# Kernel tuning notes

Hardware: AMD Instinct MI355X
Metric: run time of the kernel (lower is better)

## Reference

```python
import jax, jax.numpy as jnp
import numpy as np

DIM = 1024
N_HEADS = 16
HEAD_DIM = DIM // N_HEADS


def setup_inputs() -> dict:
    key = jax.random.key(0)
    ks = jax.random.split(key, 7)
    s = 1.0 / np.sqrt(DIM)
    return {
        "hidden_states": jax.random.normal(ks[0], (1, 4096, DIM), dtype=jnp.float32),
        "Wq": jax.random.uniform(ks[1], (DIM, DIM), jnp.float32, -s, s),
        "bq": jax.random.uniform(ks[2], (DIM,), jnp.float32, -s, s),
        "Wk": jax.random.uniform(ks[3], (DIM, DIM), jnp.float32, -s, s),
        "bk": jax.random.uniform(ks[4], (DIM,), jnp.float32, -s, s),
        "Wv": jax.random.uniform(ks[5], (DIM, DIM), jnp.float32, -s, s),
        "bv": jax.random.uniform(ks[6], (DIM,), jnp.float32, -s, s),
    }


def _split_heads(x):
    # [B, S, DIM] -> [B, H, S, HEAD_DIM]
    b, s, _ = x.shape
    return x.reshape(b, s, N_HEADS, HEAD_DIM).transpose(0, 2, 1, 3)


def reference(hidden_states, Wq, bq, Wk, bk, Wv, bv):
    q = _split_heads(hidden_states @ Wq + bq)
    k = _split_heads(hidden_states @ Wk + bk)
    v = _split_heads(hidden_states @ Wv + bv)
    scores = jnp.einsum("bhqd,bhkd->bhqk", q, k) / np.sqrt(HEAD_DIM).astype(np.float32)
    probs = jax.nn.softmax(scores, axis=-1)  # dropout prob = 0 -> identity
    ctx = jnp.einsum("bhqk,bhkd->bhqd", probs, v)
    b, h, s, d = ctx.shape
    return ctx.transpose(0, 2, 1, 3).reshape(b, s, h * d)
```

## Files before the change

### kernel.cpp

```cpp
#include <hip/hip_runtime.h>
#include <hip/hip_bf16.h>

#define S_LEN 4096
#define DIM   1024
#define NH    16
#define HD    64

typedef unsigned short u16;
typedef short  bf16x8 __attribute__((ext_vector_type(8)));
typedef float  f32x4  __attribute__((ext_vector_type(4)));

__device__ __forceinline__ u16 f2bf(float f){
  union { float f; unsigned u; } x; x.f = f;
  unsigned u = x.u;
  return (u16)((u + 0x7FFFu + ((u >> 16) & 1u)) >> 16);
}
__device__ __forceinline__ unsigned pk2(float a, float b){
  union { __hip_bfloat162 h; unsigned u; } x;
  x.h = __float22bfloat162_rn(float2{a, b});
  return x.u;
}
__device__ __forceinline__ void ld2lds16(const u16* g, u16* l){
  __builtin_amdgcn_global_load_lds((const __attribute__((address_space(1))) void*)g,
                                   (__attribute__((address_space(3))) void*)l, 16, 0, 0);
}

#define QSCALE 0.1803368801111204f

__global__ __launch_bounds__(256) void fill_sentinel(float* __restrict__ out, int n){
  int i = blockIdx.x * 256 + threadIdx.x;
  if (i < n) out[i] = 77.0f;
}

__global__ __launch_bounds__(256) void conv_x(const float* __restrict__ X, u16* __restrict__ Xb){
  size_t i = ((size_t)blockIdx.x * 256 + threadIdx.x) * 8;
  float4 v0 = *(const float4*)(X + i);
  float4 v1 = *(const float4*)(X + i + 4);
  uint4 w;
  w.x = pk2(v0.x, v0.y); w.y = pk2(v0.z, v0.w);
  w.z = pk2(v1.x, v1.y); w.w = pk2(v1.z, v1.w);
  *(uint4*)(Xb + i) = w;
}

__global__ __launch_bounds__(256) void transpose_w(
    const float* __restrict__ W0, const float* __restrict__ W1, const float* __restrict__ W2,
    u16* __restrict__ Wt)
{
  const float* W = blockIdx.z==0 ? W0 : blockIdx.z==1 ? W1 : W2;
  u16* T = Wt + (size_t)blockIdx.z * DIM * DIM;
  __shared__ __align__(16) u16 tile[64*72];
  int k0 = blockIdx.x*64, n0 = blockIdx.y*64;
  int t = threadIdx.x;
  #pragma unroll
  for (int i = 0; i < 4; ++i){
    int idx = t + i*256;
    int row = idx >> 4, col4 = (idx & 15) * 4;
    float4 v = *(const float4*)(W + (size_t)(k0+row)*DIM + n0 + col4);
    tile[(col4+0)*72 + row] = f2bf(v.x);
    tile[(col4+1)*72 + row] = f2bf(v.y);
    tile[(col4+2)*72 + row] = f2bf(v.z);
    tile[(col4+3)*72 + row] = f2bf(v.w);
  }
  __syncthreads();
  #pragma unroll
  for (int i = 0; i < 2; ++i){
    int idx = t + i*256;
    int n = idx >> 3, k16 = (idx & 7) * 8;
    *(int4*)(T + (size_t)(n0+n)*DIM + k0 + k16) = *(const int4*)(tile + n*72 + k16);
  }
}

__device__ __forceinline__ void qkv_epilogue(
    int z, int m0, int n0, int wm, int wn, int quad, int l15,
    const f32x4 acc[4][4], const float* bias,
    u16* __restrict__ qb, u16* __restrict__ kf_out, u16* __restrict__ vf_out)
{
  #pragma unroll
  for (int nt=0; nt<4; ++nt){
    int n = n0 + wn + nt*16 + l15;
    float bv = bias[n];
    int h = n >> 6, d = n & 63;
    #pragma unroll
    for (int mt=0; mt<4; ++mt){
      int mb = m0 + wm + mt*16 + quad*4;
      f32x4 c = acc[mt][nt];
      if (z == 0){
        #pragma unroll
        for (int r=0; r<4; ++r)
          qb[(size_t)(mb + r)*DIM + n] = f2bf((c[r] + bv) * QSCALE);
      } else if (z == 1){
        int half = d >> 5, quadk = (d >> 3) & 3, j = d & 7;
        #pragma unroll
        for (int r=0; r<4; ++r){
          int s = mb + r;
          size_t idx = ((((size_t)h*256 + (s >> 4))*2 + half)*64 + quadk*16 + (s & 15))*8 + j;
          kf_out[idx] = f2bf(c[r] + bv);
        }
      } else {
        int kt64 = mb >> 6;
        int kn   = (mb >> 4) & 3;
        int qsl  = (mb >> 2) & 3;
        int h2   = kn >> 1;
        int jj0  = (kn & 1) * 4;
        int dt = d >> 4, dl = d & 15;
        size_t base = (((((size_t)h*64 + kt64)*4 + dt)*2 + h2)*64 + qsl*16 + dl)*8 + jj0;
        ushort4 p;
        p.x = f2bf(c[0]+bv); p.y = f2bf(c[1]+bv);
        p.z = f2bf(c[2]+bv); p.w = f2bf(c[3]+bv);
        *(ushort4*)(vf_out + base) = p;
      }
    }
  }
}

__global__ __launch_bounds__(256) void qkv_gemm_fast(
    const u16* __restrict__ Xbf, const u16* __restrict__ Wt,
    const float* __restrict__ b0, const float* __restrict__ b1, const float* __restrict__ b2,
    u16* __restrict__ qb, u16* __restrict__ kf_out, u16* __restrict__ vf_out)
{
  int z = blockIdx.z;
  const u16* Wz = Wt + (size_t)z * DIM * DIM;
  const float* bias = z==0 ? b0 : z==1 ? b1 : b2;

  __shared__ __align__(16) u16 As[128*32];
  __shared__ __align__(16) u16 Bs[128*32];

  int m0 = blockIdx.x * 128, n0 = blockIdx.y * 128;
  int t = threadIdx.x, wave = t >> 6, lane = t & 63, quad = lane >> 4, l15 = lane & 15;
  int wm = (wave >> 1) * 64, wn = (wave & 1) * 64;

  f32x4 acc[4][4];
  #pragma unroll
  for (int i=0;i<4;++i)
    #pragma unroll
    for (int j=0;j<4;++j) acc[i][j] = (f32x4){0.f,0.f,0.f,0.f};

  int srow = wave*32 + (lane >> 2);
  int skc  = (lane & 3) * 8;
  const u16* gA0 = Xbf + (size_t)(m0 + srow)*DIM + skc;
  const u16* gA1 = gA0 + (size_t)16*DIM;
  const u16* gB0 = Wz  + (size_t)(n0 + srow)*DIM + skc;
  const u16* gB1 = gB0 + (size_t)16*DIM;
  u16* lA0 = As + srow*32 + skc;
  u16* lA1 = lA0 + 16*32;
  u16* lB0 = Bs + srow*32 + skc;
  u16* lB1 = lB0 + 16*32;

  for (int kt = 0; kt < 32; ++kt){
    int ko = kt * 32;
    __syncthreads();
    ld2lds16(gA0 + ko, lA0);
    ld2lds16(gA1 + ko, lA1);
    ld2lds16(gB0 + ko, lB0);
    ld2lds16(gB1 + ko, lB1);
    __syncthreads();
    bf16x8 af[4], bfr[4];
    #pragma unroll
    for (int mt=0; mt<4; ++mt) af[mt]  = *(const bf16x8*)(As + (wm + mt*16 + l15)*32 + quad*8);
    #pragma unroll
    for (int nt=0; nt<4; ++nt) bfr[nt] = *(const bf16x8*)(Bs + (wn + nt*16 + l15)*32 + quad*8);
    #pragma unroll
    for (int mt=0; mt<4; ++mt)
      #pragma unroll
      for (int nt=0; nt<4; ++nt)
        acc[mt][nt] = __builtin_amdgcn_mfma_f32_16x16x32_bf16(af[mt], bfr[nt], acc[mt][nt], 0, 0, 0);
  }
  qkv_epilogue(z, m0, n0, wm, wn, quad, l15, acc, bias, qb, kf_out, vf_out);
}

__global__ __launch_bounds__(256) void qkv_gemm_legacy(
    const float* __restrict__ X,
    const float* __restrict__ Wq, const float* __restrict__ Wk, const float* __restrict__ Wv,
    const float* __restrict__ b0, const float* __restrict__ b1, const float* __restrict__ b2,
    u16* __restrict__ qb, u16* __restrict__ kf_out, u16* __restrict__ vf_out)
{
  int z = blockIdx.z;
  const float* W    = z==0 ? Wq : z==1 ? Wk : Wv;
  const float* bias = z==0 ? b0 : z==1 ? b1 : b2;

  __shared__ __align__(16) u16 As[128*40];
  __shared__ __align__(16) u16 Bs[128*40];

  int m0 = blockIdx.x * 128, n0 = blockIdx.y * 128;
  int t = threadIdx.x, wave = t >> 6, lane = t & 63, quad = lane >> 4, l15 = lane & 15;
  int wm = (wave >> 1) * 64, wn = (wave & 1) * 64;

  f32x4 acc[4][4];
  #pragma unroll
  for (int i=0;i<4;++i)
    #pragma unroll
    for (int j=0;j<4;++j) acc[i][j] = (f32x4){0.f,0.f,0.f,0.f};

  int sr = t >> 2, sc = (t & 3) * 8;
  const float* gA0 = X + (size_t)(m0 + sr) * DIM + sc;
  const float* gA1 = X + (size_t)(m0 + 64 + sr) * DIM + sc;
  int br = t >> 3, bc = (t & 7) * 16;
  const float* gW = W + (size_t)br * DIM + n0 + bc;

  for (int kt = 0; kt < 32; ++kt){
    int ko = kt * 32;
    float4 a00 = *(const float4*)(gA0 + ko);
    float4 a01 = *(const float4*)(gA0 + ko + 4);
    float4 a10 = *(const float4*)(gA1 + ko);
    float4 a11 = *(const float4*)(gA1 + ko + 4);
    float4 w0  = *(const float4*)(gW + (size_t)ko*DIM);
    float4 w1  = *(const float4*)(gW + (size_t)ko*DIM + 4);
    float4 w2  = *(const float4*)(gW + (size_t)ko*DIM + 8);
    float4 w3  = *(const float4*)(gW + (size_t)ko*DIM + 12);
    int4 pa0, pa1;
    pa0.x = pk2(a00.x,a00.y); pa0.y = pk2(a00.z,a00.w);
    pa0.z = pk2(a01.x,a01.y); pa0.w = pk2(a01.z,a01.w);
    pa1.x = pk2(a10.x,a10.y); pa1.y = pk2(a10.z,a10.w);
    pa1.z = pk2(a11.x,a11.y); pa1.w = pk2(a11.z,a11.w);
    u16 wb[16];
    wb[0]=f2bf(w0.x); wb[1]=f2bf(w0.y); wb[2]=f2bf(w0.z); wb[3]=f2bf(w0.w);
    wb[4]=f2bf(w1.x); wb[5]=f2bf(w1.y); wb[6]=f2bf(w1.z); wb[7]=f2bf(w1.w);
    wb[8]=f2bf(w2.x); wb[9]=f2bf(w2.y); wb[10]=f2bf(w2.z); wb[11]=f2bf(w2.w);
    wb[12]=f2bf(w3.x); wb[13]=f2bf(w3.y); wb[14]=f2bf(w3.z); wb[15]=f2bf(w3.w);
    __syncthreads();
    *(int4*)(As + sr*40 + sc)      = pa0;
    *(int4*)(As + (64+sr)*40 + sc) = pa1;
    #pragma unroll
    for (int j=0;j<16;++j) Bs[(bc+j)*40 + br] = wb[j];
    __syncthreads();
    bf16x8 af[4], bfr[4];
    #pragma unroll
    for (int mt=0; mt<4; ++mt) af[mt]  = *(const bf16x8*)(As + (wm + mt*16 + l15)*40 + quad*8);
    #pragma unroll
    for (int nt=0; nt<4; ++nt) bfr[nt] = *(const bf16x8*)(Bs + (wn + nt*16 + l15)*40 + quad*8);
    #pragma unroll
    for (int mt=0; mt<4; ++mt)
      #pragma unroll
      for (int nt=0; nt<4; ++nt)
        acc[mt][nt] = __builtin_amdgcn_mfma_f32_16x16x32_bf16(af[mt], bfr[nt], acc[mt][nt], 0, 0, 0);
  }
  qkv_epilogue(z, m0, n0, wm, wn, quad, l15, acc, bias, qb, kf_out, vf_out);
}

__global__ __launch_bounds__(256, 2) void attn(
    const u16* __restrict__ Qb, const u16* __restrict__ Kf,
    const u16* __restrict__ Vf, float* __restrict__ out)
{
  int fid = blockIdx.x;
  int xcd  = fid & 7;
  int hpar = (fid >> 3) & 1;
  int qb   = fid >> 4;
  int h    = xcd*2 + hpar;

  int t = threadIdx.x, wave = t >> 6, lane = t & 63, quad = lane >> 4, l15 = lane & 15;
  int q0 = qb * 128 + wave * 32;

  __shared__ __align__(16) u16 Ks0[4096], Ks1[4096], Vs0[4096], Vs1[4096];

  const u16* Kfh = Kf + (size_t)h * 262144;
  const u16* Vfh = Vf + (size_t)h * 262144;

  bf16x8 qf[2][2];
  #pragma unroll
  for (int qs=0; qs<2; ++qs){
    const u16* Qp = Qb + (size_t)(q0 + qs*16 + l15)*DIM + h*HD;
    qf[qs][0] = *(const bf16x8*)(Qp + quad*8);
    qf[qs][1] = *(const bf16x8*)(Qp + 32 + quad*8);
  }

  f32x4 O[2][4];
  #pragma unroll
  for (int qs=0; qs<2; ++qs)
    #pragma unroll
    for (int dt=0; dt<4; ++dt) O[qs][dt] = (f32x4){0.f,0.f,0.f,0.f};
  float lsum[2] = {0.f, 0.f};

#define STAGE(KS, VS, T)                                                         \
  do {                                                                           \
    const u16* kg_ = Kfh + (size_t)(T)*4096 + t*8;                               \
    ld2lds16(kg_,        KS + t*8);                                              \
    ld2lds16(kg_ + 2048, KS + t*8 + 2048);                                       \
    const u16* vg_ = Vfh + (size_t)(T)*4096 + t*8;                               \
    ld2lds16(vg_,        VS + t*8);                                              \
    ld2lds16(vg_ + 2048, VS + t*8 + 2048);                                       \
  } while(0)

#define ATTN_COMPUTE(KS, VS)                                                     \
  do {                                                                           \
    bf16x8 kfr[4][2], vfr[4][2];                                                 \
    _Pragma("unroll")                                                            \
    for (int kn=0; kn<4; ++kn)                                                   \
      _Pragma("unroll")                                                          \
      for (int hf=0; hf<2; ++hf)                                                 \
        kfr[kn][hf] = *(const bf16x8*)(KS + (kn*2+hf)*512 + lane*8);             \
    _Pragma("unroll")                                                            \
    for (int dt=0; dt<4; ++dt)                                                   \
      _Pragma("unroll")                                                          \
      for (int c2=0; c2<2; ++c2)                                                 \
        vfr[dt][c2] = *(const bf16x8*)(VS + (dt*2+c2)*512 + lane*8);             \
    f32x4 st[2][4];                                                              \
    _Pragma("unroll")                                                            \
    for (int qs=0; qs<2; ++qs)                                                   \
      _Pragma("unroll")                                                          \
      for (int kn=0; kn<4; ++kn){                                                \
        f32x4 zz = (f32x4){0.f,0.f,0.f,0.f};                                     \
        zz = __builtin_amdgcn_mfma_f32_16x16x32_bf16(kfr[kn][0], qf[qs][0], zz, 0,0,0); \
        zz = __builtin_amdgcn_mfma_f32_16x16x32_bf16(kfr[kn][1], qf[qs][1], zz, 0,0,0); \
        st[qs][kn] = zz;                                                         \
      }                                                                          \
    _Pragma("unroll")                                                            \
    for (int qs=0; qs<2; ++qs){                                                  \
      float ls = 0.f;                                                            \
      _Pragma("unroll")                                                          \
      for (int kn=0; kn<4; ++kn)                                                 \
        _Pragma("unroll")                                                        \
        for (int r=0; r<4; ++r){                                                 \
          float p = __builtin_amdgcn_exp2f(st[qs][kn][r]);                       \
          st[qs][kn][r] = p; ls += p;                                            \
        }                                                                        \
      lsum[qs] += ls;                                                            \
      union { uint4 u; bf16x8 v; } pf0, pf1;                                     \
      pf0.u.x = pk2(st[qs][0][0], st[qs][0][1]);                                 \
      pf0.u.y = pk2(st[qs][0][2], st[qs][0][3]);                                 \
      pf0.u.z = pk2(st[qs][1][0], st[qs][1][1]);                                 \
      pf0.u.w = pk2(st[qs][1][2], st[qs][1][3]);                                 \
      pf1.u.x = pk2(st[qs][2][0], st[qs][2][1]);                                 \
      pf1.u.y = pk2(st[qs][2][2], st[qs][2][3]);                                 \
      pf1.u.z = pk2(st[qs][3][0], st[qs][3][1]);                                 \
      pf1.u.w = pk2(st[qs][3][2], st[qs][3][3]);                                 \
      _Pragma("unroll")                                                          \
      for (int dt=0; dt<4; ++dt){                                                \
        f32x4 o = O[qs][dt];                                                     \
        o = __builtin_amdgcn_mfma_f32_16x16x32_bf16(vfr[dt][0], pf0.v, o, 0,0,0); \
        o = __builtin_amdgcn_mfma_f32_16x16x32_bf16(vfr[dt][1], pf1.v, o, 0,0,0); \
        O[qs][dt] = o;                                                           \
      }                                                                          \
    }                                                                            \
  } while(0)

  STAGE(Ks0, Vs0, 0);
  __syncthreads();

  for (int kt = 0; kt < 64; kt += 2){
    STAGE(Ks1, Vs1, kt+1);
    ATTN_COMPUTE(Ks0, Vs0);
    __syncthreads();
    if (kt < 62) STAGE(Ks0, Vs0, kt+2);
    ATTN_COMPUTE(Ks1, Vs1);
    __syncthreads();
  }
#undef ATTN_COMPUTE
#undef STAGE

  #pragma unroll
  for (int qs=0; qs<2; ++qs){
    float l = lsum[qs];
    l += __shfl_xor(l, 16, 64);
    l += __shfl_xor(l, 32, 64);
    float inv = 1.0f / l;
    int query = q0 + qs*16 + l15;
    #pragma unroll
    for (int dt=0; dt<4; ++dt){
      float4 v;
      v.x = O[qs][dt][0]*inv; v.y = O[qs][dt][1]*inv;
      v.z = O[qs][dt][2]*inv; v.w = O[qs][dt][3]*inv;
      *(float4*)(out + (size_t)query*DIM + h*HD + dt*16 + quad*4) = v;
    }
  }
}

extern "C" void kernel_launch(void* const* d_in, const int* in_sizes, int n_in,
                              void* d_out, int out_size, void* d_ws, size_t ws_size,
                              hipStream_t stream)
{
  const float* X  = (const float*)d_in[0];
  const float* Wq = (const float*)d_in[1];
  const float* bq = (const float*)d_in[2];
  const float* Wk = (const float*)d_in[3];
  const float* bk = (const float*)d_in[4];
  const float* Wv = (const float*)d_in[5];
  const float* bv = (const float*)d_in[6];
  float* out = (float*)d_out;
  u16*   ws  = (u16*)d_ws;

  const size_t SD = (size_t)S_LEN * DIM;
  const size_t need_fast = (4*SD + 3*(size_t)DIM*DIM) * sizeof(u16);
  const size_t need_min  = (size_t)24 * 1024 * 1024;

  if (ws_size >= need_fast){
    u16* xbf = ws;
    u16* wt  = xbf + SD;
    u16* qb  = wt + 3*(size_t)DIM*DIM;
    u16* kf  = qb + SD;
    u16* vf  = kf + SD;
    conv_x       <<<dim3((int)(SD/8/256)), 256, 0, stream>>>(X, xbf);
    transpose_w  <<<dim3(16,16,3), 256, 0, stream>>>(Wq, Wk, Wv, wt);
    qkv_gemm_fast<<<dim3(32, 8, 3), 256, 0, stream>>>(xbf, wt, bq, bk, bv, qb, kf, vf);
    attn         <<<dim3(512), 256, 0, stream>>>(qb, kf, vf, out);
  } else if (ws_size >= need_min){
    u16* qb = ws;
    u16* kf = qb + SD;
    u16* vf = kf + SD;
    qkv_gemm_legacy<<<dim3(32, 8, 3), 256, 0, stream>>>(X, Wq, Wk, Wv, bq, bk, bv, qb, kf, vf);
    attn           <<<dim3(512), 256, 0, stream>>>(qb, kf, vf, out);
  } else {
    fill_sentinel<<<(out_size + 255)/256, 256, 0, stream>>>(out, out_size);
  }
}
```

Baseline: 210.9 us.

## Halve queries per wave in attention to double grid and occupancy

Each attention wave now processes one 16-query slice instead of two, so a block covers 64 queries and the grid grows to 1024 blocks, with launch bounds raised to allow 4 blocks per CU. This lowers register pressure and raises occupancy to hide latency of the exp and MFMA chain. In exchange, each staged K/V tile is reused by half as many queries, doubling K/V load and LDS traffic per unit of work.

```diff
diff --git a/kernel.cpp b/kernel.cpp
--- a/kernel.cpp
+++ b/kernel.cpp
@@ -237,7 +237,7 @@
   qkv_epilogue(z, m0, n0, wm, wn, quad, l15, acc, bias, qb, kf_out, vf_out);
 }
 
-__global__ __launch_bounds__(256, 2) void attn(
+__global__ __launch_bounds__(256, 4) void attn(
     const u16* __restrict__ Qb, const u16* __restrict__ Kf,
     const u16* __restrict__ Vf, float* __restrict__ out)
 {
@@ -248,27 +248,24 @@
   int h    = xcd*2 + hpar;
 
   int t = threadIdx.x, wave = t >> 6, lane = t & 63, quad = lane >> 4, l15 = lane & 15;
-  int q0 = qb * 128 + wave * 32;
+  int q0 = qb * 64 + wave * 16;
 
   __shared__ __align__(16) u16 Ks0[4096], Ks1[4096], Vs0[4096], Vs1[4096];
 
   const u16* Kfh = Kf + (size_t)h * 262144;
   const u16* Vfh = Vf + (size_t)h * 262144;
 
-  bf16x8 qf[2][2];
-  #pragma unroll
-  for (int qs=0; qs<2; ++qs){
-    const u16* Qp = Qb + (size_t)(q0 + qs*16 + l15)*DIM + h*HD;
-    qf[qs][0] = *(const bf16x8*)(Qp + quad*8);
-    qf[qs][1] = *(const bf16x8*)(Qp + 32 + quad*8);
-  }
-
-  f32x4 O[2][4];
-  #pragma unroll
-  for (int qs=0; qs<2; ++qs)
-    #pragma unroll
-    for (int dt=0; dt<4; ++dt) O[qs][dt] = (f32x4){0.f,0.f,0.f,0.f};
-  float lsum[2] = {0.f, 0.f};
+  bf16x8 qf[2];
+  {
+    const u16* Qp = Qb + (size_t)(q0 + l15)*DIM + h*HD;
+    qf[0] = *(const bf16x8*)(Qp + quad*8);
+    qf[1] = *(const bf16x8*)(Qp + 32 + quad*8);
+  }
+
+  f32x4 O[4];
+  #pragma unroll
+  for (int dt=0; dt<4; ++dt) O[dt] = (f32x4){0.f,0.f,0.f,0.f};
+  float lsum = 0.f;
 
 #define STAGE(KS, VS, T)                                                         \
   do {                                                                           \
@@ -293,43 +290,38 @@
       _Pragma("unroll")                                                          \
       for (int c2=0; c2<2; ++c2)                                                 \
         vfr[dt][c2] = *(const bf16x8*)(VS + (dt*2+c2)*512 + lane*8);             \
-    f32x4 st[2][4];                                                              \
-    _Pragma("unroll")                                                            \
-    for (int qs=0; qs<2; ++qs)                                                   \
+    f32x4 st[4];                                                                 \
+    _Pragma("unroll")                                                            \
+    for (int kn=0; kn<4; ++kn){                                                  \
+      f32x4 zz = (f32x4){0.f,0.f,0.f,0.f};                                       \
+      zz = __builtin_amdgcn_mfma_f32_16x16x32_bf16(kfr[kn][0], qf[0], zz, 0,0,0); \
+      zz = __builtin_amdgcn_mfma_f32_16x16x32_bf16(kfr[kn][1], qf[1], zz, 0,0,0); \
+      st[kn] = zz;                                                               \
+    }                                                                            \
+    float ls = 0.f;                                                              \
+    _Pragma("unroll")                                                            \
+    for (int kn=0; kn<4; ++kn)                                                   \
       _Pragma("unroll")                                                          \
-      for (int kn=0; kn<4; ++kn){                                                \
-        f32x4 zz = (f32x4){0.f,0.f,0.f,0.f};                                     \
-        zz = __builtin_amdgcn_mfma_f32_16x16x32_bf16(kfr[kn][0], qf[qs][0], zz, 0,0,0); \
-        zz = __builtin_amdgcn_mfma_f32_16x16x32_bf16(kfr[kn][1], qf[qs][1], zz, 0,0,0); \
-        st[qs][kn] = zz;                                                         \
+      for (int r=0; r<4; ++r){                                                   \
+        float p = __builtin_amdgcn_exp2f(st[kn][r]);                             \
+        st[kn][r] = p; ls += p;                                                  \
       }                                                                          \
-    _Pragma("unroll")                                                            \
-    for (int qs=0; qs<2; ++qs){                                                  \
-      float ls = 0.f;                                                            \
-      _Pragma("unroll")                                                          \
-      for (int kn=0; kn<4; ++kn)                                                 \
-        _Pragma("unroll")                                                        \
-        for (int r=0; r<4; ++r){                                                 \
-          float p = __builtin_amdgcn_exp2f(st[qs][kn][r]);                       \
-          st[qs][kn][r] = p; ls += p;                                            \
-        }                                                                        \
-      lsum[qs] += ls;                                                            \
-      union { uint4 u; bf16x8 v; } pf0, pf1;                                     \
-      pf0.u.x = pk2(st[qs][0][0], st[qs][0][1]);                                 \
-      pf0.u.y = pk2(st[qs][0][2], st[qs][0][3]);                                 \
-      pf0.u.z = pk2(st[qs][1][0], st[qs][1][1]);                                 \
-      pf0.u.w = pk2(st[qs][1][2], st[qs][1][3]);                                 \
-      pf1.u.x = pk2(st[qs][2][0], st[qs][2][1]);                                 \
-      pf1.u.y = pk2(st[qs][2][2], st[qs][2][3]);                                 \
-      pf1.u.z = pk2(st[qs][3][0], st[qs][3][1]);                                 \
-      pf1.u.w = pk2(st[qs][3][2], st[qs][3][3]);                                 \
-      _Pragma("unroll")                                                          \
-      for (int dt=0; dt<4; ++dt){                                                \
-        f32x4 o = O[qs][dt];                                                     \
-        o = __builtin_amdgcn_mfma_f32_16x16x32_bf16(vfr[dt][0], pf0.v, o, 0,0,0); \
-        o = __builtin_amdgcn_mfma_f32_16x16x32_bf16(vfr[dt][1], pf1.v, o, 0,0,0); \
-        O[qs][dt] = o;                                                           \
-      }                                                                          \
+    lsum += ls;                                                                  \
+    union { uint4 u; bf16x8 v; } pf0, pf1;                                       \
+    pf0.u.x = pk2(st[0][0], st[0][1]);                                           \
+    pf0.u.y = pk2(st[0][2], st[0][3]);                                           \
+    pf0.u.z = pk2(st[1][0], st[1][1]);                                           \
+    pf0.u.w = pk2(st[1][2], st[1][3]);                                           \
+    pf1.u.x = pk2(st[2][0], st[2][1]);                                           \
+    pf1.u.y = pk2(st[2][2], st[2][3]);                                           \
+    pf1.u.z = pk2(st[3][0], st[3][1]);                                           \
+    pf1.u.w = pk2(st[3][2], st[3][3]);                                           \
+    _Pragma("unroll")                                                            \
+    for (int dt=0; dt<4; ++dt){                                                  \
+      f32x4 o = O[dt];                                                           \
+      o = __builtin_amdgcn_mfma_f32_16x16x32_bf16(vfr[dt][0], pf0.v, o, 0,0,0);  \
+      o = __builtin_amdgcn_mfma_f32_16x16x32_bf16(vfr[dt][1], pf1.v, o, 0,0,0);  \
+      O[dt] = o;                                                                 \
     }                                                                            \
   } while(0)
 
@@ -347,18 +339,17 @@
 #undef ATTN_COMPUTE
 #undef STAGE
 
-  #pragma unroll
-  for (int qs=0; qs<2; ++qs){
-    float l = lsum[qs];
+  {
+    float l = lsum;
     l += __shfl_xor(l, 16, 64);
     l += __shfl_xor(l, 32, 64);
     float inv = 1.0f / l;
-    int query = q0 + qs*16 + l15;
+    int query = q0 + l15;
     #pragma unroll
     for (int dt=0; dt<4; ++dt){
       float4 v;
-      v.x = O[qs][dt][0]*inv; v.y = O[qs][dt][1]*inv;
-      v.z = O[qs][dt][2]*inv; v.w = O[qs][dt][3]*inv;
+      v.x = O[dt][0]*inv; v.y = O[dt][1]*inv;
+      v.z = O[dt][2]*inv; v.w = O[dt][3]*inv;
       *(float4*)(out + (size_t)query*DIM + h*HD + dt*16 + quad*4) = v;
     }
   }
@@ -391,13 +382,13 @@
     conv_x       <<<dim3((int)(SD/8/256)), 256, 0, stream>>>(X, xbf);
     transpose_w  <<<dim3(16,16,3), 256, 0, stream>>>(Wq, Wk, Wv, wt);
     qkv_gemm_fast<<<dim3(32, 8, 3), 256, 0, stream>>>(xbf, wt, bq, bk, bv, qb, kf, vf);
-    attn         <<<dim3(512), 256, 0, stream>>>(qb, kf, vf, out);
+    attn         <<<dim3(1024), 256, 0, stream>>>(qb, kf, vf, out);
   } else if (ws_size >= need_min){
     u16* qb = ws;
     u16* kf = qb + SD;
     u16* vf = kf + SD;
     qkv_gemm_legacy<<<dim3(32, 8, 3), 256, 0, stream>>>(X, Wq, Wk, Wv, bq, bk, bv, qb, kf, vf);
-    attn           <<<dim3(512), 256, 0, stream>>>(qb, kf, vf, out);
+    attn           <<<dim3(1024), 256, 0, stream>>>(qb, kf, vf, out);
   } else {
     fill_sentinel<<<(out_size + 255)/256, 256, 0, stream>>>(out, out_size);
   }
```

After: 213.9 us. Within noise of the previous version (+1.4%).

## Software-pipeline attention loop to overlap QK of next tile with PV of previous

Applied to the files above, without the earlier changes.

Restructures the attention inner loop so that the QK^T MFMAs for tile t+1 are issued alongside the PV MFMAs for tile t, with exp/pack and V-fragment loads done one stage ahead in registers. The aim is to hide the dependency chain between score computation, exp, and the PV matmul, and to let matrix work overlap with transcendental work. It adds double-buffered register state (scores, packed probs, V fragments), which raises register pressure and could cut occupancy.

```diff
diff --git a/kernel.cpp b/kernel.cpp
--- a/kernel.cpp
+++ b/kernel.cpp
@@ -280,20 +280,14 @@
     ld2lds16(vg_ + 2048, VS + t*8 + 2048);                                       \
   } while(0)
 
-#define ATTN_COMPUTE(KS, VS)                                                     \
+#define QK_BLOCK(KS, ST)                                                         \
   do {                                                                           \
-    bf16x8 kfr[4][2], vfr[4][2];                                                 \
+    bf16x8 kfr[4][2];                                                            \
     _Pragma("unroll")                                                            \
     for (int kn=0; kn<4; ++kn)                                                   \
       _Pragma("unroll")                                                          \
       for (int hf=0; hf<2; ++hf)                                                 \
-        kfr[kn][hf] = *(const bf16x8*)(KS + (kn*2+hf)*512 + lane*8);             \
-    _Pragma("unroll")                                                            \
-    for (int dt=0; dt<4; ++dt)                                                   \
-      _Pragma("unroll")                                                          \
-      for (int c2=0; c2<2; ++c2)                                                 \
-        vfr[dt][c2] = *(const bf16x8*)(VS + (dt*2+c2)*512 + lane*8);             \
-    f32x4 st[2][4];                                                              \
+        kfr[kn][hf] = *(const bf16x8*)((KS) + (kn*2+hf)*512 + lane*8);           \
     _Pragma("unroll")                                                            \
     for (int qs=0; qs<2; ++qs)                                                   \
       _Pragma("unroll")                                                          \
@@ -301,8 +295,25 @@
         f32x4 zz = (f32x4){0.f,0.f,0.f,0.f};                                     \
         zz = __builtin_amdgcn_mfma_f32_16x16x32_bf16(kfr[kn][0], qf[qs][0], zz, 0,0,0); \
         zz = __builtin_amdgcn_mfma_f32_16x16x32_bf16(kfr[kn][1], qf[qs][1], zz, 0,0,0); \
-        st[qs][kn] = zz;                                                         \
+        ST[qs][kn] = zz;                                                         \
       }                                                                          \
+  } while(0)
+
+#define PV_BLOCK(PF, VFR)                                                        \
+  do {                                                                           \
+    _Pragma("unroll")                                                            \
+    for (int qs=0; qs<2; ++qs)                                                   \
+      _Pragma("unroll")                                                          \
+      for (int dt=0; dt<4; ++dt){                                                \
+        f32x4 o = O[qs][dt];                                                     \
+        o = __builtin_amdgcn_mfma_f32_16x16x32_bf16(VFR[dt][0], PF[qs][0].v, o, 0,0,0); \
+        o = __builtin_amdgcn_mfma_f32_16x16x32_bf16(VFR[dt][1], PF[qs][1].v, o, 0,0,0); \
+        O[qs][dt] = o;                                                           \
+      }                                                                          \
+  } while(0)
+
+#define EXP_PACK(ST, PF)                                                         \
+  do {                                                                           \
     _Pragma("unroll")                                                            \
     for (int qs=0; qs<2; ++qs){                                                  \
       float ls = 0.f;                                                            \
@@ -310,42 +321,73 @@
       for (int kn=0; kn<4; ++kn)                                                 \
         _Pragma("unroll")                                                        \
         for (int r=0; r<4; ++r){                                                 \
-          float p = __builtin_amdgcn_exp2f(st[qs][kn][r]);                       \
-          st[qs][kn][r] = p; ls += p;                                            \
+          float p = __builtin_amdgcn_exp2f(ST[qs][kn][r]);                       \
+          ST[qs][kn][r] = p; ls += p;                                            \
         }                                                                        \
       lsum[qs] += ls;                                                            \
-      union { uint4 u; bf16x8 v; } pf0, pf1;                                     \
-      pf0.u.x = pk2(st[qs][0][0], st[qs][0][1]);                                 \
-      pf0.u.y = pk2(st[qs][0][2], st[qs][0][3]);                                 \
-      pf0.u.z = pk2(st[qs][1][0], st[qs][1][1]);                                 \
-      pf0.u.w = pk2(st[qs][1][2], st[qs][1][3]);                                 \
-      pf1.u.x = pk2(st[qs][2][0], st[qs][2][1]);                                 \
-      pf1.u.y = pk2(st[qs][2][2], st[qs][2][3]);                                 \
-      pf1.u.z = pk2(st[qs][3][0], st[qs][3][1]);                                 \
-      pf1.u.w = pk2(st[qs][3][2], st[qs][3][3]);                                 \
-      _Pragma("unroll")                                                          \
-      for (int dt=0; dt<4; ++dt){                                                \
-        f32x4 o = O[qs][dt];                                                     \
-        o = __builtin_amdgcn_mfma_f32_16x16x32_bf16(vfr[dt][0], pf0.v, o, 0,0,0); \
-        o = __builtin_amdgcn_mfma_f32_16x16x32_bf16(vfr[dt][1], pf1.v, o, 0,0,0); \
-        O[qs][dt] = o;                                                           \
-      }                                                                          \
+      PF[qs][0].u.x = pk2(ST[qs][0][0], ST[qs][0][1]);                           \
+      PF[qs][0].u.y = pk2(ST[qs][0][2], ST[qs][0][3]);                           \
+      PF[qs][0].u.z = pk2(ST[qs][1][0], ST[qs][1][1]);                           \
+      PF[qs][0].u.w = pk2(ST[qs][1][2], ST[qs][1][3]);                           \
+      PF[qs][1].u.x = pk2(ST[qs][2][0], ST[qs][2][1]);                           \
+      PF[qs][1].u.y = pk2(ST[qs][2][2], ST[qs][2][3]);                           \
+      PF[qs][1].u.z = pk2(ST[qs][3][0], ST[qs][3][1]);                           \
+      PF[qs][1].u.w = pk2(ST[qs][3][2], ST[qs][3][3]);                           \
     }                                                                            \
   } while(0)
 
+#define LOADV(VFR, VS)                                                           \
+  do {                                                                           \
+    _Pragma("unroll")                                                            \
+    for (int dt=0; dt<4; ++dt)                                                   \
+      _Pragma("unroll")                                                          \
+      for (int c2=0; c2<2; ++c2)                                                 \
+        VFR[dt][c2] = *(const bf16x8*)((VS) + (dt*2+c2)*512 + lane*8);           \
+  } while(0)
+
+  typedef union { uint4 u; bf16x8 v; } pfu;
+  pfu pfA[2][2], pfB[2][2];
+  bf16x8 vfrA[4][2], vfrB[4][2];
+  f32x4 stA[2][4], stB[2][4];
+
   STAGE(Ks0, Vs0, 0);
   __syncthreads();
-
-  for (int kt = 0; kt < 64; kt += 2){
-    STAGE(Ks1, Vs1, kt+1);
-    ATTN_COMPUTE(Ks0, Vs0);
-    __syncthreads();
-    if (kt < 62) STAGE(Ks0, Vs0, kt+2);
-    ATTN_COMPUTE(Ks1, Vs1);
-    __syncthreads();
-  }
-#undef ATTN_COMPUTE
+  STAGE(Ks1, Vs1, 1);
+  QK_BLOCK(Ks0, stA);
+  EXP_PACK(stA, pfA);
+  LOADV(vfrA, Vs0);
+  __syncthreads();
+
+  for (int i = 0; i < 31; ++i){
+    int t1 = 2*i + 1;
+    {
+      STAGE(Ks0, Vs0, t1+1);
+      QK_BLOCK(Ks1, stB);
+      PV_BLOCK(pfA, vfrA);
+      EXP_PACK(stB, pfB);
+      LOADV(vfrB, Vs1);
+      __syncthreads();
+    }
+    {
+      STAGE(Ks1, Vs1, t1+2);
+      QK_BLOCK(Ks0, stA);
+      PV_BLOCK(pfB, vfrB);
+      EXP_PACK(stA, pfA);
+      LOADV(vfrA, Vs0);
+      __syncthreads();
+    }
+  }
+  QK_BLOCK(Ks1, stB);
+  PV_BLOCK(pfA, vfrA);
+  EXP_PACK(stB, pfB);
+  LOADV(vfrB, Vs1);
+  PV_BLOCK(pfB, vfrB);
+
 #undef STAGE
+#undef QK_BLOCK
+#undef PV_BLOCK
+#undef EXP_PACK
+#undef LOADV
 
   #pragma unroll
   for (int qs=0; qs<2; ++qs){
```

After: 208.4 us. Within noise of the previous version (-1.2%).

## Stagger waves between QK/exp and PV phases with software pipelining and setprio

Applied to the files above, without the earlier changes.

Splits the attention tile compute into QK+exp, V load and PV steps. Half of the waves, chosen by wave parity XOR block index, defer the PV of the previous tile so it runs before the current QK. This staggers which phase different waves are in, so exp/VALU work in one wave can overlap MFMA work in another. It also raises wave priority around the MFMA sections. The cost is extra registers for the carried P fragments and V fragments, which may hurt occupancy at launch bounds of 2 blocks per CU, and the control flow becomes divergent per wave.

```diff
diff --git a/kernel.cpp b/kernel.cpp
--- a/kernel.cpp
+++ b/kernel.cpp
@@ -249,6 +249,7 @@
 
   int t = threadIdx.x, wave = t >> 6, lane = t & 63, quad = lane >> 4, l15 = lane & 15;
   int q0 = qb * 128 + wave * 32;
+  int dg = (wave ^ (fid >> 8)) & 1;
 
   __shared__ __align__(16) u16 Ks0[4096], Ks1[4096], Vs0[4096], Vs1[4096];
 
@@ -269,6 +270,8 @@
     #pragma unroll
     for (int dt=0; dt<4; ++dt) O[qs][dt] = (f32x4){0.f,0.f,0.f,0.f};
   float lsum[2] = {0.f, 0.f};
+
+  typedef union { uint4 u; bf16x8 v; } pfu;
 
 #define STAGE(KS, VS, T)                                                         \
   do {                                                                           \
@@ -280,20 +283,16 @@
     ld2lds16(vg_ + 2048, VS + t*8 + 2048);                                       \
   } while(0)
 
-#define ATTN_COMPUTE(KS, VS)                                                     \
+#define QK_EXP(KS, PF)                                                           \
   do {                                                                           \
-    bf16x8 kfr[4][2], vfr[4][2];                                                 \
+    bf16x8 kfr[4][2];                                                            \
     _Pragma("unroll")                                                            \
     for (int kn=0; kn<4; ++kn)                                                   \
       _Pragma("unroll")                                                          \
       for (int hf=0; hf<2; ++hf)                                                 \
-        kfr[kn][hf] = *(const bf16x8*)(KS + (kn*2+hf)*512 + lane*8);             \
-    _Pragma("unroll")                                                            \
-    for (int dt=0; dt<4; ++dt)                                                   \
-      _Pragma("unroll")                                                          \
-      for (int c2=0; c2<2; ++c2)                                                 \
-        vfr[dt][c2] = *(const bf16x8*)(VS + (dt*2+c2)*512 + lane*8);             \
+        kfr[kn][hf] = *(const bf16x8*)((KS) + (kn*2+hf)*512 + lane*8);           \
     f32x4 st[2][4];                                                              \
+    __builtin_amdgcn_s_setprio(1);                                               \
     _Pragma("unroll")                                                            \
     for (int qs=0; qs<2; ++qs)                                                   \
       _Pragma("unroll")                                                          \
@@ -303,6 +302,7 @@
         zz = __builtin_amdgcn_mfma_f32_16x16x32_bf16(kfr[kn][1], qf[qs][1], zz, 0,0,0); \
         st[qs][kn] = zz;                                                         \
       }                                                                          \
+    __builtin_amdgcn_s_setprio(0);                                               \
     _Pragma("unroll")                                                            \
     for (int qs=0; qs<2; ++qs){                                                  \
       float ls = 0.f;                                                            \
@@ -314,38 +314,80 @@
           st[qs][kn][r] = p; ls += p;                                            \
         }                                                                        \
       lsum[qs] += ls;                                                            \
-      union { uint4 u; bf16x8 v; } pf0, pf1;                                     \
-      pf0.u.x = pk2(st[qs][0][0], st[qs][0][1]);                                 \
-      pf0.u.y = pk2(st[qs][0][2], st[qs][0][3]);                                 \
-      pf0.u.z = pk2(st[qs][1][0], st[qs][1][1]);                                 \
-      pf0.u.w = pk2(st[qs][1][2], st[qs][1][3]);                                 \
-      pf1.u.x = pk2(st[qs][2][0], st[qs][2][1]);                                 \
-      pf1.u.y = pk2(st[qs][2][2], st[qs][2][3]);                                 \
-      pf1.u.z = pk2(st[qs][3][0], st[qs][3][1]);                                 \
-      pf1.u.w = pk2(st[qs][3][2], st[qs][3][3]);                                 \
+      PF[qs][0].u.x = pk2(st[qs][0][0], st[qs][0][1]);                           \
+      PF[qs][0].u.y = pk2(st[qs][0][2], st[qs][0][3]);                           \
+      PF[qs][0].u.z = pk2(st[qs][1][0], st[qs][1][1]);                           \
+      PF[qs][0].u.w = pk2(st[qs][1][2], st[qs][1][3]);                           \
+      PF[qs][1].u.x = pk2(st[qs][2][0], st[qs][2][1]);                           \
+      PF[qs][1].u.y = pk2(st[qs][2][2], st[qs][2][3]);                           \
+      PF[qs][1].u.z = pk2(st[qs][3][0], st[qs][3][1]);                           \
+      PF[qs][1].u.w = pk2(st[qs][3][2], st[qs][3][3]);                           \
+    }                                                                            \
+  } while(0)
+
+#define LOADV(VFR, VS)                                                           \
+  do {                                                                           \
+    _Pragma("unroll")                                                            \
+    for (int dt=0; dt<4; ++dt)                                                   \
+      _Pragma("unroll")                                                          \
+      for (int c2=0; c2<2; ++c2)                                                 \
+        VFR[dt][c2] = *(const bf16x8*)((VS) + (dt*2+c2)*512 + lane*8);           \
+  } while(0)
+
+#define PV(PF, VFR)                                                              \
+  do {                                                                           \
+    __builtin_amdgcn_s_setprio(1);                                               \
+    _Pragma("unroll")                                                            \
+    for (int qs=0; qs<2; ++qs)                                                   \
       _Pragma("unroll")                                                          \
       for (int dt=0; dt<4; ++dt){                                                \
         f32x4 o = O[qs][dt];                                                     \
-        o = __builtin_amdgcn_mfma_f32_16x16x32_bf16(vfr[dt][0], pf0.v, o, 0,0,0); \
-        o = __builtin_amdgcn_mfma_f32_16x16x32_bf16(vfr[dt][1], pf1.v, o, 0,0,0); \
+        o = __builtin_amdgcn_mfma_f32_16x16x32_bf16(VFR[dt][0], PF[qs][0].v, o, 0,0,0); \
+        o = __builtin_amdgcn_mfma_f32_16x16x32_bf16(VFR[dt][1], PF[qs][1].v, o, 0,0,0); \
         O[qs][dt] = o;                                                           \
       }                                                                          \
+    __builtin_amdgcn_s_setprio(0);                                               \
+  } while(0)
+
+#define COMPUTE(KS, VS, FIRST)                                                   \
+  do {                                                                           \
+    if (!dg){                                                                    \
+      pfu pfN[2][2]; bf16x8 vfrN[4][2];                                          \
+      QK_EXP(KS, pfN);                                                           \
+      LOADV(vfrN, VS);                                                           \
+      PV(pfN, vfrN);                                                             \
+    } else {                                                                     \
+      if (!(FIRST)) PV(pfC, vfrC);                                               \
+      QK_EXP(KS, pfC);                                                           \
+      LOADV(vfrC, VS);                                                           \
     }                                                                            \
   } while(0)
 
+  pfu pfC[2][2];
+  bf16x8 vfrC[4][2];
+
   STAGE(Ks0, Vs0, 0);
   __syncthreads();
-
-  for (int kt = 0; kt < 64; kt += 2){
-    STAGE(Ks1, Vs1, kt+1);
-    ATTN_COMPUTE(Ks0, Vs0);
-    __syncthreads();
-    if (kt < 62) STAGE(Ks0, Vs0, kt+2);
-    ATTN_COMPUTE(Ks1, Vs1);
-    __syncthreads();
-  }
-#undef ATTN_COMPUTE
+  STAGE(Ks1, Vs1, 1);
+  COMPUTE(Ks0, Vs0, 1);
+  __syncthreads();
+
+  for (int kt = 1; kt < 63; kt += 2){
+    STAGE(Ks0, Vs0, kt+1);
+    COMPUTE(Ks1, Vs1, 0);
+    __syncthreads();
+    STAGE(Ks1, Vs1, kt+2);
+    COMPUTE(Ks0, Vs0, 0);
+    __syncthreads();
+  }
+  COMPUTE(Ks1, Vs1, 0);
+  if (dg) PV(pfC, vfrC);
+
 #undef STAGE
+#undef QK_EXP
+#undef LOADV
+#undef PV
+#undef COMPUTE
 
   #pragma unroll
   for (int qs=0; qs<2; ++qs){
```

Measured after the change: 210.0 us. Within noise of the previous version (-0.5%).
